# Kernel optimization log

Measured on AMD Instinct MI355X. Metric: run time of the kernel, lower is better.

Reference implementation:

```python
import jax, jax.numpy as jnp
import numpy as np

B, S, HID = 4, 2048, 1024
NH, NKV, HD = 16, 4, 64
GROUPS = NH // NKV
SCALE = HD ** -0.5


def make_rope(seq_len, dim, base=10000.0):
    inv_freq = 1.0 / (base ** (np.arange(0, dim, 2, dtype=np.float32) / dim))
    t = np.arange(seq_len, dtype=np.float32)
    freqs = np.outer(t, inv_freq)                      # [S, D/2]
    emb = np.concatenate([freqs, freqs], axis=-1)      # [S, D] duplicated-half convention
    cos = jnp.asarray(np.cos(emb))[None, None]         # [1,1,S,D]
    sin = jnp.asarray(np.sin(emb))[None, None]
    return cos, sin


def setup_inputs() -> dict:
    key = jax.random.key(0)
    ks = jax.random.split(key, 8)
    hidden_states = jax.random.normal(ks[0], (B, S, HID), dtype=jnp.float32)
    cos, sin = make_rope(S, HD)
    std = HID ** -0.5
    Wq = jax.random.normal(ks[1], (NH * HD, HID), dtype=jnp.float32) * std
    bq = jnp.zeros((NH * HD,), dtype=jnp.float32)
    Wk = jax.random.normal(ks[2], (NKV * HD, HID), dtype=jnp.float32) * std
    bk = jnp.zeros((NKV * HD,), dtype=jnp.float32)
    Wv = jax.random.normal(ks[3], (NKV * HD, HID), dtype=jnp.float32) * std
    bv = jnp.zeros((NKV * HD,), dtype=jnp.float32)
    Wo = jax.random.normal(ks[4], (HID, NH * HD), dtype=jnp.float32) * std
    bo = jnp.zeros((HID,), dtype=jnp.float32)
    return dict(hidden_states=hidden_states, cos=cos, sin=sin,
                Wq=Wq, bq=bq, Wk=Wk, bk=bk, Wv=Wv, bv=bv, Wo=Wo, bo=bo)


def rotate_half(x):
    x1, x2 = jnp.split(x, 2, axis=-1)
    return jnp.concatenate([-x2, x1], axis=-1)


def reference(hidden_states, cos, sin, Wq, bq, Wk, bk, Wv, bv, Wo, bo):
    x = hidden_states  # [B,S,HID]
    q = (x @ Wq.T + bq).reshape(B, S, NH, HD).transpose(0, 2, 1, 3)    # [B,NH,S,D]
    k = (x @ Wk.T + bk).reshape(B, S, NKV, HD).transpose(0, 2, 1, 3)   # [B,NKV,S,D]
    v = (x @ Wv.T + bv).reshape(B, S, NKV, HD).transpose(0, 2, 1, 3)
    # RoPE
    q = q * cos + rotate_half(q) * sin
    k = k * cos + rotate_half(k) * sin
    # GQA: repeat_interleave kv heads to match q heads
    k = jnp.repeat(k, GROUPS, axis=1)  # [B,NH,S,D]
    v = jnp.repeat(v, GROUPS, axis=1)
    # scaled dot-product attention (no mask, no dropout at eval)
    scores = jnp.einsum('bhqd,bhkd->bhqk', q, k) * SCALE
    attn = jax.nn.softmax(scores, axis=-1)
    out = jnp.einsum('bhqk,bhkd->bhqd', attn, v)       # [B,NH,S,D]
    out = out.transpose(0, 2, 1, 3).reshape(B, S, NH * HD)
    return out @ Wo.T + bo
```

## Files before the change

kernel.cpp:

```cpp
#include <hip/hip_runtime.h>
#include <stdint.h>

#define S_LEN 2048
#define HIDDEN 1024
#define NHEADS 16
#define NKVH 4
#define HDIM 64

typedef __bf16 bf16x8 __attribute__((ext_vector_type(8)));
typedef __bf16 bf16x4 __attribute__((ext_vector_type(4)));
typedef float f32x4 __attribute__((ext_vector_type(4)));
typedef short s16x4 __attribute__((ext_vector_type(4)));
typedef unsigned short U16;

#define OFF_XB   0u
#define OFF_WQB  8388608u
#define OFF_WKB  9437184u
#define OFF_WVB  9699328u
#define OFF_WOB  9961472u
#define OFF_Q    11010048u
#define OFF_K    19398656u
#define OFF_V    21495808u
#define OFF_AWS  OFF_XB

static __device__ __forceinline__ U16 f2bf(float f){
    unsigned u;
    __builtin_memcpy(&u, &f, 4);
    u += 0x7FFFu + ((u >> 16) & 1u);
    return (U16)(u >> 16);
}
static __device__ __forceinline__ uint32_t pkbf(float lo, float hi){
    uint32_t a, b;
    __builtin_memcpy(&a, &lo, 4); a += 0x7FFFu + ((a >> 16) & 1u);
    __builtin_memcpy(&b, &hi, 4); b += 0x7FFFu + ((b >> 16) & 1u);
    return (a >> 16) | (b & 0xFFFF0000u);
}

typedef __attribute__((address_space(3))) uint32_t lds_u32;
typedef const __attribute__((address_space(1))) uint32_t glb_u32;
static __device__ __forceinline__ void glds16(const U16* g, U16* l){
    __builtin_amdgcn_global_load_lds((glb_u32*)g, (lds_u32*)l, 16, 0, 0);
}

__global__ void conv_kernel(const float* __restrict__ X,  const float* __restrict__ Wq,
                            const float* __restrict__ Wk, const float* __restrict__ Wv,
                            const float* __restrict__ Wo, U16* __restrict__ dst)
{
    size_t i4 = (size_t)blockIdx.x * 256 + threadIdx.x;
    size_t e = i4 * 4;
    const float* s;
    if (e < 8388608u)       s = X  + e;
    else if (e < 9437184u)  s = Wq + (e - 8388608u);
    else if (e < 9699328u)  s = Wk + (e - 9437184u);
    else if (e < 9961472u)  s = Wv + (e - 9699328u);
    else                    s = Wo + (e - 9961472u);
    float4 v = *(const float4*)s;
    uint2 o; o.x = pkbf(v.x, v.y); o.y = pkbf(v.z, v.w);
    *(uint2*)(dst + e) = o;
}

__global__ __launch_bounds__(256, 3)
void qkv_kernel(const U16* __restrict__ Xb,
                const U16* __restrict__ Wqb, const U16* __restrict__ Wkb, const U16* __restrict__ Wvb,
                const float* __restrict__ bq, const float* __restrict__ bk, const float* __restrict__ bv,
                const float* __restrict__ cosT, const float* __restrict__ sinT,
                U16* __restrict__ qws, U16* __restrict__ kws, U16* __restrict__ vtws)
{
    __shared__ __align__(16) U16 Asm[128 * 64];
    __shared__ __align__(16) U16 Bsm[128 * 64];

    const int mblk = blockIdx.x;
    const int nblk = blockIdx.y;
    const int tid  = threadIdx.x;
    const int wave = tid >> 6, lane = tid & 63;
    const int ln = lane & 15, quad = lane >> 4;
    const int wm = wave >> 1, wn = wave & 1;

    const U16* Wp; const float* biasp; int region;
    const int nbase = nblk * 128;
    if (nblk < 8)       { Wp = Wqb + (size_t)nbase * HIDDEN;          biasp = bq + nbase;          region = 0; }
    else if (nblk < 10) { Wp = Wkb + (size_t)(nbase - 1024) * HIDDEN; biasp = bk + (nbase - 1024); region = 1; }
    else                { Wp = Wvb + (size_t)(nbase - 1280) * HIDDEN; biasp = bv + (nbase - 1280); region = 2; }
    const U16* Xp = Xb + (size_t)mblk * 128 * HIDDEN;

    f32x4 acc[4][4];
    #pragma unroll
    for (int i = 0; i < 4; i++)
        #pragma unroll
        for (int j = 0; j < 4; j++) acc[i][j] = (f32x4){0.f, 0.f, 0.f, 0.f};

    const int l8 = lane >> 3;
    const int cg = (lane & 7) ^ l8;
    const int sw = ln & 7;

    #pragma unroll
    for (int t = 0; t < 4; t++) {
        int rbase = wave * 32 + t * 8;
        glds16(Xp + (size_t)(rbase + l8) * HIDDEN + cg * 8, &Asm[rbase * 64]);
        glds16(Wp + (size_t)(rbase + l8) * HIDDEN + cg * 8, &Bsm[rbase * 64]);
    }

    for (int k0 = 0; k0 < HIDDEN; k0 += 64) {
        __syncthreads();

        bf16x8 af[4][2], bfr[4][2];
        #pragma unroll
        for (int i = 0; i < 4; i++)
            #pragma unroll
            for (int ks = 0; ks < 2; ks++) {
                af[i][ks]  = *(const bf16x8*)(&Asm[(wm * 64 + i * 16 + ln) * 64 + (((ks * 4 + quad) ^ sw) * 8)]);
                bfr[i][ks] = *(const bf16x8*)(&Bsm[(wn * 64 + i * 16 + ln) * 64 + (((ks * 4 + quad) ^ sw) * 8)]);
            }
        __syncthreads();

        if (k0 + 64 < HIDDEN) {
            #pragma unroll
            for (int t = 0; t < 4; t++) {
                int rbase = wave * 32 + t * 8;
                glds16(Xp + (size_t)(rbase + l8) * HIDDEN + (k0 + 64) + cg * 8, &Asm[rbase * 64]);
                glds16(Wp + (size_t)(rbase + l8) * HIDDEN + (k0 + 64) + cg * 8, &Bsm[rbase * 64]);
            }
        }
        __builtin_amdgcn_sched_barrier(0);

        #pragma unroll
        for (int i = 0; i < 4; i++)
            #pragma unroll
            for (int j = 0; j < 4; j++) {
                acc[i][j] = __builtin_amdgcn_mfma_f32_16x16x32_bf16(af[i][0], bfr[j][0], acc[i][j], 0, 0, 0);
                acc[i][j] = __builtin_amdgcn_mfma_f32_16x16x32_bf16(af[i][1], bfr[j][1], acc[i][j], 0, 0, 0);
            }
    }

    float bias[4];
    #pragma unroll
    for (int j = 0; j < 4; j++) bias[j] = biasp[wn * 64 + j * 16 + ln];

    const float QSCALE = 0.125f * 1.44269504089f;

    if (region == 2) {
        #pragma unroll
        for (int i = 0; i < 4; i++) {
            int m0 = mblk * 128 + wm * 64 + i * 16 + quad * 4;
            int b = m0 >> 11;
            int st6 = m0 & (S_LEN - 1);
            int tile = st6 >> 6, soff = st6 & 63;
            #pragma unroll
            for (int j = 0; j < 4; j++) {
                int n2 = nbase - 1280 + wn * 64 + j * 16 + ln;
                int hh = n2 >> 6, d = n2 & 63;
                uint2 w;
                w.x = pkbf(acc[i][j][0] + bias[j], acc[i][j][1] + bias[j]);
                w.y = pkbf(acc[i][j][2] + bias[j], acc[i][j][3] + bias[j]);
                *(uint2*)(vtws + ((((size_t)b * NKVH + hh) * 32 + tile) * 64 + d) * 64 + soff) = w;
            }
        }
    } else {
        #pragma unroll
        for (int i = 0; i < 4; i++) {
            #pragma unroll
            for (int r = 0; r < 4; r++) {
                int m = mblk * 128 + wm * 64 + i * 16 + quad * 4 + r;
                int s = m & (S_LEN - 1), b = m >> 11;
                float vals[4];
                #pragma unroll
                for (int j = 0; j < 4; j++) vals[j] = acc[i][j][r] + bias[j];
                const float* cb = cosT + s * HDIM;
                const float* sb = sinT + s * HDIM;
                float c0 = cb[ln],      c1 = cb[16 + ln];
                float s0 = sb[ln],      s1 = sb[16 + ln];
                float outv[4];
                outv[0] = vals[0] * c0 - vals[2] * s0;
                outv[1] = vals[1] * c1 - vals[3] * s1;
                outv[2] = vals[2] * c0 + vals[0] * s0;
                outv[3] = vals[3] * c1 + vals[1] * s1;
                if (region == 0) {
                    #pragma unroll
                    for (int j = 0; j < 4; j++) {
                        int n = nbase + wn * 64 + j * 16 + ln;
                        int hh = n >> 6, d = n & 63;
                        qws[(((size_t)b * NHEADS + hh) * S_LEN + s) * HDIM + d] = f2bf(outv[j] * QSCALE);
                    }
                } else {
                    #pragma unroll
                    for (int j = 0; j < 4; j++) {
                        int n2 = nbase - 1024 + wn * 64 + j * 16 + ln;
                        int hh = n2 >> 6, d = n2 & 63;
                        kws[(((size_t)b * NKVH + hh) * S_LEN + s) * HDIM + d] = f2bf(outv[j]);
                    }
                }
            }
        }
    }
}

__global__ __launch_bounds__(256, 4)
void attn_kernel(const U16* __restrict__ qws, const U16* __restrict__ kws,
                 const U16* __restrict__ vtws, U16* __restrict__ aws)
{
    __shared__ __align__(16) U16 Ksm[2][64 * 64];
    __shared__ __align__(16) U16 VTsm[2][64 * 64];

    const int qt = blockIdx.x;
    const int hg = blockIdx.y;
    const int b = hg >> 4, h = hg & 15, hkv = h >> 2;
    const U16* Qh  = qws  + (size_t)hg * S_LEN * HDIM;
    const U16* Kh  = kws  + (size_t)(b * NKVH + hkv) * S_LEN * HDIM;
    const U16* VTh = vtws + (size_t)(b * NKVH + hkv) * HDIM * S_LEN;

    const int tid = threadIdx.x;
    const int wave = tid >> 6, lane = tid & 63;
    const int ln = lane & 15, quad = lane >> 4;
    const int sw = ln & 7;
    const int voff = (quad & 1) * 4;

    bf16x8 qf[2][2];
    #pragma unroll
    for (int i = 0; i < 2; i++)
        #pragma unroll
        for (int ks = 0; ks < 2; ks++) {
            int row = qt * 128 + wave * 32 + i * 16 + ln;
            qf[i][ks] = *(const bf16x8*)(Qh + (size_t)row * HDIM + ks * 32 + quad * 8);
        }

    float rsA[2] = {0.f, 0.f}, rsB[2] = {0.f, 0.f};
    f32x4 o_t[4][2];
    #pragma unroll
    for (int n = 0; n < 4; n++)
        #pragma unroll
        for (int i = 0; i < 2; i++) o_t[n][i] = (f32x4){0.f, 0.f, 0.f, 0.f};

    const int l8 = lane >> 3;
    const int cgk = (lane & 7) ^ l8;

    const int koff0 = ln * 64 + ((quad ^ sw) * 8);
    const int koff1 = ln * 64 + (((quad + 4) ^ sw) * 8);
    const int vbase = ln * 64 + voff;
    int cvo[4];
    #pragma unroll
    for (int j = 0; j < 4; j++) cvo[j] = (((j * 2 + (quad >> 1)) ^ sw) * 8);

    const U16* pk[2]; const U16* pv[2];
    U16* dK[2]; U16* dV[2];
    #pragma unroll
    for (int t = 0; t < 2; t++) {
        int c = wave * 2 + t;
        pk[t] = Kh  + (size_t)(c * 8 + l8) * HDIM + cgk * 8;
        pv[t] = VTh + (size_t)(c * 8 + l8) * 64  + cgk * 8;
        dK[t] = &Ksm[0][c * 8 * 64];
        dV[t] = &VTsm[0][c * 8 * 64];
    }

    #pragma unroll
    for (int t = 0; t < 2; t++) {
        glds16(pk[t], dK[t]);
        glds16(pv[t], dV[t]);
        pk[t] += 4096; pv[t] += 4096;
    }

    s16x4 pfp[2];
    pfp[0] = (s16x4){0, 0, 0, 0}; pfp[1] = (s16x4){0, 0, 0, 0};
    s16x4 vfp[4];
    #pragma unroll
    for (int n = 0; n < 4; n++) vfp[n] = (s16x4){0, 0, 0, 0};

    int p = 0;
    for (int kt = 0; kt < 32; kt++) {
        __syncthreads();

        if (kt < 31) {
            #pragma unroll
            for (int t = 0; t < 2; t++) {
                glds16(pk[t], dK[t] + (p ^ 1) * 4096);
                glds16(pv[t], dV[t] + (p ^ 1) * 4096);
                pk[t] += 4096; pv[t] += 4096;
            }
        }

        const U16* Kb = &Ksm[p][0];
        const U16* Vb = &VTsm[p][0];

        bf16x8 kfa = *(const bf16x8*)(Kb + koff0);
        bf16x8 kfb = *(const bf16x8*)(Kb + koff1);

        #pragma unroll
        for (int j = 0; j < 4; j++) {
            __builtin_amdgcn_s_setprio(1);
            f32x4 z[2];
            #pragma unroll
            for (int i = 0; i < 2; i++) {
                z[i] = (f32x4){0.f, 0.f, 0.f, 0.f};
                z[i] = __builtin_amdgcn_mfma_f32_16x16x32_bf16(kfa, qf[i][0], z[i], 0, 0, 0);
                z[i] = __builtin_amdgcn_mfma_f32_16x16x32_bf16(kfb, qf[i][1], z[i], 0, 0, 0);
            }
            #pragma unroll
            for (int n = 0; n < 4; n++)
                #pragma unroll
                for (int i = 0; i < 2; i++)
                    o_t[n][i] = __builtin_amdgcn_mfma_f32_16x16x16bf16_1k(vfp[n], pfp[i], o_t[n][i], 0, 0, 0);
            __builtin_amdgcn_s_setprio(0);

            if (j < 3) {
                kfa = *(const bf16x8*)(Kb + (j + 1) * 1024 + koff0);
                kfb = *(const bf16x8*)(Kb + (j + 1) * 1024 + koff1);
            }
            s16x4 vf[4];
            const U16* Vj = Vb + vbase + cvo[j];
            #pragma unroll
            for (int n = 0; n < 4; n++)
                vf[n] = *(const s16x4*)(Vj + n * 1024);
            __builtin_amdgcn_sched_barrier(0);

            s16x4 pf[2];
            #pragma unroll
            for (int i = 0; i < 2; i++) {
                bf16x4 pb;
                #pragma unroll
                for (int r = 0; r < 4; r++) {
                    float pe = __builtin_amdgcn_exp2f(z[i][r]);
                    if (r & 1) rsB[i] += pe; else rsA[i] += pe;
                    pb[r] = (__bf16)pe;
                }
                __builtin_memcpy(&pf[i], &pb, 8);
            }
            #pragma unroll
            for (int n = 0; n < 4; n++) vfp[n] = vf[n];
            pfp[0] = pf[0]; pfp[1] = pf[1];
        }
        p ^= 1;
    }

    #pragma unroll
    for (int n = 0; n < 4; n++)
        #pragma unroll
        for (int i = 0; i < 2; i++)
            o_t[n][i] = __builtin_amdgcn_mfma_f32_16x16x16bf16_1k(vfp[n], pfp[i], o_t[n][i], 0, 0, 0);

    float inv_li[2];
    #pragma unroll
    for (int i = 0; i < 2; i++) {
        float t = rsA[i] + rsB[i];
        t += __shfl_xor(t, 16);
        t += __shfl_xor(t, 32);
        inv_li[i] = 1.f / t;
    }
    #pragma unroll
    for (int n = 0; n < 4; n++)
        #pragma unroll
        for (int i = 0; i < 2; i++) {
            int q = qt * 128 + wave * 32 + i * 16 + ln;
            int d = n * 16 + quad * 4;
            uint2 w;
            w.x = pkbf(o_t[n][i][0] * inv_li[i], o_t[n][i][1] * inv_li[i]);
            w.y = pkbf(o_t[n][i][2] * inv_li[i], o_t[n][i][3] * inv_li[i]);
            *(uint2*)(aws + ((size_t)b * S_LEN + q) * (NHEADS * HDIM) + h * HDIM + d) = w;
        }
}

__global__ __launch_bounds__(256, 3)
void proj_kernel(const U16* __restrict__ A, const U16* __restrict__ Wob,
                 const float* __restrict__ bo, float* __restrict__ out)
{
    __shared__ __align__(16) U16 Asm[128 * 64];
    __shared__ __align__(16) U16 Bsm[128 * 64];

    const int mblk = blockIdx.x;
    const int nblk = blockIdx.y;
    const int tid  = threadIdx.x;
    const int wave = tid >> 6, lane = tid & 63;
    const int ln = lane & 15, quad = lane >> 4;
    const int wm = wave >> 1, wn = wave & 1;

    const int nbase = nblk * 128;
    const U16* Wp = Wob + (size_t)nbase * HIDDEN;
    const U16* Ap = A + (size_t)mblk * 128 * HIDDEN;

    f32x4 acc[4][4];
    #pragma unroll
    for (int i = 0; i < 4; i++)
        #pragma unroll
        for (int j = 0; j < 4; j++) acc[i][j] = (f32x4){0.f, 0.f, 0.f, 0.f};

    const int l8 = lane >> 3;
    const int cg = (lane & 7) ^ l8;
    const int sw = ln & 7;

    #pragma unroll
    for (int t = 0; t < 4; t++) {
        int rbase = wave * 32 + t * 8;
        glds16(Ap + (size_t)(rbase + l8) * HIDDEN + cg * 8, &Asm[rbase * 64]);
        glds16(Wp + (size_t)(rbase + l8) * HIDDEN + cg * 8, &Bsm[rbase * 64]);
    }

    for (int k0 = 0; k0 < HIDDEN; k0 += 64) {
        __syncthreads();

        bf16x8 af[4][2], bfr[4][2];
        #pragma unroll
        for (int i = 0; i < 4; i++)
            #pragma unroll
            for (int ks = 0; ks < 2; ks++) {
                af[i][ks]  = *(const bf16x8*)(&Asm[(wm * 64 + i * 16 + ln) * 64 + (((ks * 4 + quad) ^ sw) * 8)]);
                bfr[i][ks] = *(const bf16x8*)(&Bsm[(wn * 64 + i * 16 + ln) * 64 + (((ks * 4 + quad) ^ sw) * 8)]);
            }
        __syncthreads();

        if (k0 + 64 < HIDDEN) {
            #pragma unroll
            for (int t = 0; t < 4; t++) {
                int rbase = wave * 32 + t * 8;
                glds16(Ap + (size_t)(rbase + l8) * HIDDEN + (k0 + 64) + cg * 8, &Asm[rbase * 64]);
                glds16(Wp + (size_t)(rbase + l8) * HIDDEN + (k0 + 64) + cg * 8, &Bsm[rbase * 64]);
            }
        }
        __builtin_amdgcn_sched_barrier(0);

        #pragma unroll
        for (int i = 0; i < 4; i++)
            #pragma unroll
            for (int j = 0; j < 4; j++) {
                acc[i][j] = __builtin_amdgcn_mfma_f32_16x16x32_bf16(af[i][0], bfr[j][0], acc[i][j], 0, 0, 0);
                acc[i][j] = __builtin_amdgcn_mfma_f32_16x16x32_bf16(af[i][1], bfr[j][1], acc[i][j], 0, 0, 0);
            }
    }

    float bias[4];
    #pragma unroll
    for (int j = 0; j < 4; j++) bias[j] = bo[nbase + wn * 64 + j * 16 + ln];

    #pragma unroll
    for (int i = 0; i < 4; i++)
        #pragma unroll
        for (int r = 0; r < 4; r++) {
            int m = mblk * 128 + wm * 64 + i * 16 + quad * 4 + r;
            #pragma unroll
            for (int j = 0; j < 4; j++) {
                int n = nbase + wn * 64 + j * 16 + ln;
                out[(size_t)m * HIDDEN + n] = acc[i][j][r] + bias[j];
            }
        }
}

extern "C" void kernel_launch(void* const* d_in, const int* in_sizes, int n_in,
                              void* d_out, int out_size, void* d_ws, size_t ws_size,
                              hipStream_t stream)
{
    const float* X    = (const float*)d_in[0];
    const float* cosT = (const float*)d_in[1];
    const float* sinT = (const float*)d_in[2];
    const float* Wq   = (const float*)d_in[3];
    const float* bq   = (const float*)d_in[4];
    const float* Wk   = (const float*)d_in[5];
    const float* bk   = (const float*)d_in[6];
    const float* Wv   = (const float*)d_in[7];
    const float* bv   = (const float*)d_in[8];
    const float* Wo   = (const float*)d_in[9];
    const float* bo   = (const float*)d_in[10];
    float* out = (float*)d_out;

    U16* wsb = (U16*)d_ws;
    U16* Xb   = wsb + OFF_XB;
    U16* Wqb  = wsb + OFF_WQB;
    U16* Wkb  = wsb + OFF_WKB;
    U16* Wvb  = wsb + OFF_WVB;
    U16* Wob  = wsb + OFF_WOB;
    U16* qws  = wsb + OFF_Q;
    U16* kws  = wsb + OFF_K;
    U16* vtws = wsb + OFF_V;
    U16* aws  = wsb + OFF_AWS;

    conv_kernel<<<dim3(10752), 256, 0, stream>>>(X, Wq, Wk, Wv, Wo, wsb);
    qkv_kernel<<<dim3(64, 12), 256, 0, stream>>>(Xb, Wqb, Wkb, Wvb, bq, bk, bv, cosT, sinT, qws, kws, vtws);
    attn_kernel<<<dim3(16, 64), 256, 0, stream>>>(qws, kws, vtws, aws);
    proj_kernel<<<dim3(64, 8), 256, 0, stream>>>(aws, Wob, bo, out);
}
```

Baseline: 242.8 us.

## Double-buffer LDS tiles in QKV and output projection GEMMs

Both projection GEMMs now use two LDS buffers per operand, so the next K-tile can be loaded while the current one is read and multiplied. This removes the second barrier per iteration and lets global loads overlap the LDS fragment reads and MFMAs. In exchange, shared memory per block doubles and launch bounds drop to two blocks per CU, which reduces occupancy.

```diff
diff --git a/kernel.cpp b/kernel.cpp
--- a/kernel.cpp
+++ b/kernel.cpp
@@ -59,15 +59,15 @@
     *(uint2*)(dst + e) = o;
 }
 
-__global__ __launch_bounds__(256, 3)
+__global__ __launch_bounds__(256, 2)
 void qkv_kernel(const U16* __restrict__ Xb,
                 const U16* __restrict__ Wqb, const U16* __restrict__ Wkb, const U16* __restrict__ Wvb,
                 const float* __restrict__ bq, const float* __restrict__ bk, const float* __restrict__ bv,
                 const float* __restrict__ cosT, const float* __restrict__ sinT,
                 U16* __restrict__ qws, U16* __restrict__ kws, U16* __restrict__ vtws)
 {
-    __shared__ __align__(16) U16 Asm[128 * 64];
-    __shared__ __align__(16) U16 Bsm[128 * 64];
+    __shared__ __align__(16) U16 Asm[2][128 * 64];
+    __shared__ __align__(16) U16 Bsm[2][128 * 64];
 
     const int mblk = blockIdx.x;
     const int nblk = blockIdx.y;
@@ -96,33 +96,32 @@
     #pragma unroll
     for (int t = 0; t < 4; t++) {
         int rbase = wave * 32 + t * 8;
-        glds16(Xp + (size_t)(rbase + l8) * HIDDEN + cg * 8, &Asm[rbase * 64]);
-        glds16(Wp + (size_t)(rbase + l8) * HIDDEN + cg * 8, &Bsm[rbase * 64]);
-    }
-
+        glds16(Xp + (size_t)(rbase + l8) * HIDDEN + cg * 8, &Asm[0][rbase * 64]);
+        glds16(Wp + (size_t)(rbase + l8) * HIDDEN + cg * 8, &Bsm[0][rbase * 64]);
+    }
+
+    int p = 0;
     for (int k0 = 0; k0 < HIDDEN; k0 += 64) {
         __syncthreads();
 
-        bf16x8 af[4][2], bfr[4][2];
-        #pragma unroll
-        for (int i = 0; i < 4; i++)
-            #pragma unroll
-            for (int ks = 0; ks < 2; ks++) {
-                af[i][ks]  = *(const bf16x8*)(&Asm[(wm * 64 + i * 16 + ln) * 64 + (((ks * 4 + quad) ^ sw) * 8)]);
-                bfr[i][ks] = *(const bf16x8*)(&Bsm[(wn * 64 + i * 16 + ln) * 64 + (((ks * 4 + quad) ^ sw) * 8)]);
-            }
-        __syncthreads();
-
         if (k0 + 64 < HIDDEN) {
             #pragma unroll
             for (int t = 0; t < 4; t++) {
                 int rbase = wave * 32 + t * 8;
-                glds16(Xp + (size_t)(rbase + l8) * HIDDEN + (k0 + 64) + cg * 8, &Asm[rbase * 64]);
-                glds16(Wp + (size_t)(rbase + l8) * HIDDEN + (k0 + 64) + cg * 8, &Bsm[rbase * 64]);
+                glds16(Xp + (size_t)(rbase + l8) * HIDDEN + (k0 + 64) + cg * 8, &Asm[p ^ 1][rbase * 64]);
+                glds16(Wp + (size_t)(rbase + l8) * HIDDEN + (k0 + 64) + cg * 8, &Bsm[p ^ 1][rbase * 64]);
             }
         }
         __builtin_amdgcn_sched_barrier(0);
 
+        bf16x8 af[4][2], bfr[4][2];
+        #pragma unroll
+        for (int i = 0; i < 4; i++)
+            #pragma unroll
+            for (int ks = 0; ks < 2; ks++) {
+                af[i][ks]  = *(const bf16x8*)(&Asm[p][(wm * 64 + i * 16 + ln) * 64 + (((ks * 4 + quad) ^ sw) * 8)]);
+                bfr[i][ks] = *(const bf16x8*)(&Bsm[p][(wn * 64 + i * 16 + ln) * 64 + (((ks * 4 + quad) ^ sw) * 8)]);
+            }
         #pragma unroll
         for (int i = 0; i < 4; i++)
             #pragma unroll
@@ -130,6 +129,7 @@
                 acc[i][j] = __builtin_amdgcn_mfma_f32_16x16x32_bf16(af[i][0], bfr[j][0], acc[i][j], 0, 0, 0);
                 acc[i][j] = __builtin_amdgcn_mfma_f32_16x16x32_bf16(af[i][1], bfr[j][1], acc[i][j], 0, 0, 0);
             }
+        p ^= 1;
     }
 
     float bias[4];
@@ -357,12 +357,12 @@
         }
 }
 
-__global__ __launch_bounds__(256, 3)
+__global__ __launch_bounds__(256, 2)
 void proj_kernel(const U16* __restrict__ A, const U16* __restrict__ Wob,
                  const float* __restrict__ bo, float* __restrict__ out)
 {
-    __shared__ __align__(16) U16 Asm[128 * 64];
-    __shared__ __align__(16) U16 Bsm[128 * 64];
+    __shared__ __align__(16) U16 Asm[2][128 * 64];
+    __shared__ __align__(16) U16 Bsm[2][128 * 64];
 
     const int mblk = blockIdx.x;
     const int nblk = blockIdx.y;
@@ -388,33 +388,32 @@
     #pragma unroll
     for (int t = 0; t < 4; t++) {
         int rbase = wave * 32 + t * 8;
-        glds16(Ap + (size_t)(rbase + l8) * HIDDEN + cg * 8, &Asm[rbase * 64]);
-        glds16(Wp + (size_t)(rbase + l8) * HIDDEN + cg * 8, &Bsm[rbase * 64]);
-    }
-
+        glds16(Ap + (size_t)(rbase + l8) * HIDDEN + cg * 8, &Asm[0][rbase * 64]);
+        glds16(Wp + (size_t)(rbase + l8) * HIDDEN + cg * 8, &Bsm[0][rbase * 64]);
+    }
+
+    int p = 0;
     for (int k0 = 0; k0 < HIDDEN; k0 += 64) {
         __syncthreads();
 
-        bf16x8 af[4][2], bfr[4][2];
-        #pragma unroll
-        for (int i = 0; i < 4; i++)
-            #pragma unroll
-            for (int ks = 0; ks < 2; ks++) {
-                af[i][ks]  = *(const bf16x8*)(&Asm[(wm * 64 + i * 16 + ln) * 64 + (((ks * 4 + quad) ^ sw) * 8)]);
-                bfr[i][ks] = *(const bf16x8*)(&Bsm[(wn * 64 + i * 16 + ln) * 64 + (((ks * 4 + quad) ^ sw) * 8)]);
-            }
-        __syncthreads();
-
         if (k0 + 64 < HIDDEN) {
             #pragma unroll
             for (int t = 0; t < 4; t++) {
                 int rbase = wave * 32 + t * 8;
-                glds16(Ap + (size_t)(rbase + l8) * HIDDEN + (k0 + 64) + cg * 8, &Asm[rbase * 64]);
-                glds16(Wp + (size_t)(rbase + l8) * HIDDEN + (k0 + 64) + cg * 8, &Bsm[rbase * 64]);
+                glds16(Ap + (size_t)(rbase + l8) * HIDDEN + (k0 + 64) + cg * 8, &Asm[p ^ 1][rbase * 64]);
+                glds16(Wp + (size_t)(rbase + l8) * HIDDEN + (k0 + 64) + cg * 8, &Bsm[p ^ 1][rbase * 64]);
             }
         }
         __builtin_amdgcn_sched_barrier(0);
 
+        bf16x8 af[4][2], bfr[4][2];
+        #pragma unroll
+        for (int i = 0; i < 4; i++)
+            #pragma unroll
+            for (int ks = 0; ks < 2; ks++) {
+                af[i][ks]  = *(const bf16x8*)(&Asm[p][(wm * 64 + i * 16 + ln) * 64 + (((ks * 4 + quad) ^ sw) * 8)]);
+                bfr[i][ks] = *(const bf16x8*)(&Bsm[p][(wn * 64 + i * 16 + ln) * 64 + (((ks * 4 + quad) ^ sw) * 8)]);
+            }
         #pragma unroll
         for (int i = 0; i < 4; i++)
             #pragma unroll
@@ -422,6 +421,7 @@
                 acc[i][j] = __builtin_amdgcn_mfma_f32_16x16x32_bf16(af[i][0], bfr[j][0], acc[i][j], 0, 0, 0);
                 acc[i][j] = __builtin_amdgcn_mfma_f32_16x16x32_bf16(af[i][1], bfr[j][1], acc[i][j], 0, 0, 0);
             }
+        p ^= 1;
     }
 
     float bias[4];
```

After: 261.7 us. 1.08x slower.
